# Kernel optimization log

Hardware: AMD Instinct MI355X
Metric: run time of the kernel (lower is better)

## Reference

```python
import jax, jax.numpy as jnp
import numpy as np

D_MODEL = 1024
NUM_HEADS = 16
HEAD_DIM = D_MODEL // NUM_HEADS


def setup_inputs() -> dict:
    key = jax.random.key(0)
    ks = jax.random.split(key, 5)
    x = jax.random.normal(ks[0], (4, 2048, D_MODEL), dtype=jnp.float32)
    # xavier_uniform with gain=0.1 for square (D,D) weights: limit = 0.1*sqrt(6/(D+D))
    limit = 0.1 * np.sqrt(6.0 / (2 * D_MODEL))
    def w(k):
        return jax.random.uniform(k, (D_MODEL, D_MODEL), jnp.float32, -limit, limit)
    return {
        "x": x,
        "W_q": w(ks[1]), "b_q": jnp.zeros((D_MODEL,), jnp.float32),
        "W_k": w(ks[2]), "b_k": jnp.zeros((D_MODEL,), jnp.float32),
        "W_v": w(ks[3]), "b_v": jnp.zeros((D_MODEL,), jnp.float32),
        "W_o": w(ks[4]), "b_o": jnp.zeros((D_MODEL,), jnp.float32),
    }


def reference(x, W_q, b_q, W_k, b_k, W_v, b_v, W_o, b_o):
    B, S, D = x.shape
    H, Hd = NUM_HEADS, HEAD_DIM
    # Linear: x @ W^T + b (torch nn.Linear convention); weights here are (out, in)
    def proj(W, b):
        y = jnp.einsum('bsd,ed->bse', x, W) + b
        return y.reshape(B, S, H, Hd).transpose(0, 2, 1, 3)  # [B,H,S,Hd]
    Q = proj(W_q, b_q)
    K = proj(W_k, b_k)
    V = proj(W_v, b_v)
    scale = 1.0 / np.sqrt(Hd).astype(np.float32)
    scores = jnp.einsum('bhqd,bhkd->bhqk', Q, K) * scale  # [B,H,S,S]
    attn = jax.nn.softmax(scores, axis=-1)
    ctx = jnp.einsum('bhqk,bhkd->bhqd', attn, V)
    ctx = ctx.transpose(0, 2, 1, 3).reshape(B, S, D)
    out = jnp.einsum('bsd,ed->bse', ctx, W_o) + b_o
    return out
```

## Files before the change

kernel.cpp:

```cpp
#include <hip/hip_runtime.h>
#include <math.h>

#define B_  4
#define S_  2048
#define D_  1024
#define H_  16
#define HD_ 64
#define M_  (B_*S_)

typedef short short8 __attribute__((ext_vector_type(8)));
typedef float f32x4 __attribute__((ext_vector_type(4)));

#define MFMA16(a,b,c) __builtin_amdgcn_mfma_f32_16x16x32_bf16(a, b, c, 0, 0, 0)

#if __has_builtin(__builtin_amdgcn_exp2f)
#define EXP2(x) __builtin_amdgcn_exp2f(x)
#else
#define EXP2(x) exp2f(x)
#endif

__device__ __forceinline__ unsigned short f2bf(float f) {
    unsigned u = __float_as_uint(f);
    u = (u + 0x7FFF + ((u >> 16) & 1)) >> 16;
    return (unsigned short)u;
}

__device__ __forceinline__ unsigned pack_bf16(float a, float b) {
#if __has_builtin(__builtin_amdgcn_cvt_pk_bf16_f32)
    typedef __bf16 bf2 __attribute__((ext_vector_type(2)));
    bf2 v = __builtin_amdgcn_cvt_pk_bf16_f32(a, b);
    unsigned r;
    __builtin_memcpy(&r, &v, 4);
    return r;
#else
    unsigned ua = __float_as_uint(a), ub = __float_as_uint(b);
    ua += 0x7FFFu + ((ua >> 16) & 1u);
    ub += 0x7FFFu + ((ub >> 16) & 1u);
    return __builtin_amdgcn_perm(ub, ua, 0x07060302u);
#endif
}

__device__ __forceinline__ void async_copy16(const void* g, void* l) {
    __builtin_amdgcn_global_load_lds(
        (const __attribute__((address_space(1))) void*)g,
        (__attribute__((address_space(3))) void*)l, 16, 0, 0);
}

#define VMW(n) asm volatile("s_waitcnt vmcnt(" #n ")" ::: "memory")
#define BARS() do { __builtin_amdgcn_s_barrier(); \
                    __builtin_amdgcn_sched_barrier(0); } while (0)

__global__ __launch_bounds__(256) void cvt_all(
    const float* __restrict__ x,
    const float* __restrict__ w0, const float* __restrict__ w1,
    const float* __restrict__ w2, const float* __restrict__ w3,
    unsigned short* __restrict__ xb, unsigned short* __restrict__ wb)
{
    size_t i = ((size_t)blockIdx.x * 256 + threadIdx.x) * 4;
    const float* src; unsigned short* dst;
    if (i < (size_t)M_ * D_) {
        src = x + i; dst = xb + i;
    } else {
        size_t j = i - (size_t)M_ * D_;
        int z = (int)(j >> 20);
        const float* w = (z == 0) ? w0 : (z == 1) ? w1 : (z == 2) ? w2 : w3;
        src = w + (j & ((size_t)D_ * D_ - 1)); dst = wb + j;
    }
    float4 v = *(const float4*)src;
    uint2 o;
    o.x = pack_bf16(v.x, v.y);
    o.y = pack_bf16(v.z, v.w);
    *(uint2*)dst = o;
}

__global__ __launch_bounds__(512, 2) void qkv256(
    const unsigned short* __restrict__ A,
    const unsigned short* __restrict__ W,
    const float* __restrict__ bq, const float* __restrict__ bk,
    const float* __restrict__ bv,
    unsigned short* __restrict__ Qo, unsigned short* __restrict__ Ko,
    unsigned short* __restrict__ Vo)
{
    __shared__ unsigned short As[2][256 * 64];
    __shared__ unsigned short Ws[2][256 * 64];
    const int K = D_;
    int tid = threadIdx.x;
    int w = tid >> 6, lane = tid & 63;
    int quad = lane >> 4, l16 = lane & 15;
    int r8 = lane >> 3, c8 = lane & 7;
    int cK = c8 ^ r8;
    int wm = w >> 2, wn = w & 3;
    int fl = l16 & 7;

    int lin = blockIdx.x + 12 * blockIdx.y;
    int swz = (lin & 7) * 48 + (lin >> 3);
    int by = swz / 12, bx = swz % 12;
    int m0 = by * 256, n0 = bx * 256;

    int z = bx >> 2;
    const float* bias = (z == 0) ? bq : (z == 1) ? bk : bv;
    unsigned short* out = (z == 0) ? Qo : (z == 1) ? Ko : Vo;
    float cscale = (z == 0) ? 0.125f * 1.44269504088896f : 1.0f;

    f32x4 acc[8][4];
    #pragma unroll
    for (int i = 0; i < 8; ++i)
        #pragma unroll
        for (int j = 0; j < 4; ++j)
            acc[i][j] = (f32x4){0.f, 0.f, 0.f, 0.f};

    const unsigned short* Ag = A + (size_t)(m0 + r8) * K + cK * 8;
    const unsigned short* Wg = W + (size_t)(n0 + r8) * K + cK * 8;

    auto stA = [&](int slot, int kt, int h) {
        #pragma unroll
        for (int ii = 0; ii < 2; ++ii) {
            int rb = ii * 128 + h * 64 + w * 8;
            async_copy16(Ag + (size_t)rb * K + kt * 64, &As[slot][rb * 64]);
        }
    };
    auto stB = [&](int slot, int kt, int h) {
        #pragma unroll
        for (int ii = 0; ii < 2; ++ii) {
            int rb = (ii * 2 + (w >> 2)) * 64 + h * 32 + (w & 3) * 8;
            async_copy16(Wg + (size_t)rb * K + kt * 64, &Ws[slot][rb * 64]);
        }
    };

    stA(0, 0, 0); stB(0, 0, 0); stB(0, 0, 1); stA(0, 0, 1);
    VMW(4);
    BARS();

    #define RD_A(i, off, s) (*(const short8*)&As[cur][(wm * 128 + (off) + (i) * 16 + l16) * 64 + \
                              (((quad + (s) * 4) ^ fl) * 8)])
    #define RD_B(j, off, s) (*(const short8*)&Ws[cur][(wn * 64 + (off) + (j) * 16 + l16) * 64 + \
                              (((quad + (s) * 4) ^ fl) * 8)])

    const int NT = K / 64;
    for (int kt = 0; kt < NT; ++kt) {
        int cur = kt & 1, nxt = cur ^ 1;
        bool pre = (kt + 1 < NT);
        short8 a[4][2], b0[2][2], b1[2][2];

        #pragma unroll
        for (int i = 0; i < 4; ++i)
            #pragma unroll
            for (int s = 0; s < 2; ++s) a[i][s] = RD_A(i, 0, s);
        #pragma unroll
        for (int j = 0; j < 2; ++j)
            #pragma unroll
            for (int s = 0; s < 2; ++s) b0[j][s] = RD_B(j, 0, s);
        if (pre) { stA(nxt, kt + 1, 0); VMW(4); } else VMW(2);
        BARS();
        #pragma unroll
        for (int i = 0; i < 4; ++i)
            #pragma unroll
            for (int j = 0; j < 2; ++j)
                #pragma unroll
                for (int s = 0; s < 2; ++s)
                    acc[i][j] = MFMA16(a[i][s], b0[j][s], acc[i][j]);

        #pragma unroll
        for (int j = 0; j < 2; ++j)
            #pragma unroll
            for (int s = 0; s < 2; ++s) b1[j][s] = RD_B(j, 32, s);
        if (pre) { stB(nxt, kt + 1, 0); VMW(4); } else VMW(0);
        BARS();
        #pragma unroll
        for (int i = 0; i < 4; ++i)
            #pragma unroll
            for (int j = 0; j < 2; ++j)
                #pragma unroll
                for (int s = 0; s < 2; ++s)
                    acc[i][j + 2] = MFMA16(a[i][s], b1[j][s], acc[i][j + 2]);

        #pragma unroll
        for (int i = 0; i < 4; ++i)
            #pragma unroll
            for (int s = 0; s < 2; ++s) a[i][s] = RD_A(i, 64, s);
        if (pre) stB(nxt, kt + 1, 1);
        BARS();
        #pragma unroll
        for (int i = 0; i < 4; ++i)
            #pragma unroll
            for (int j = 0; j < 2; ++j)
                #pragma unroll
                for (int s = 0; s < 2; ++s)
                    acc[i + 4][j + 2] = MFMA16(a[i][s], b1[j][s], acc[i + 4][j + 2]);

        if (pre) { stA(nxt, kt + 1, 1); VMW(4); }
        BARS();
        #pragma unroll
        for (int i = 0; i < 4; ++i)
            #pragma unroll
            for (int j = 0; j < 2; ++j)
                #pragma unroll
                for (int s = 0; s < 2; ++s)
                    acc[i + 4][j] = MFMA16(a[i][s], b0[j][s], acc[i + 4][j]);
    }
    #undef RD_A
    #undef RD_B

    #pragma unroll
    for (int ih = 0; ih < 2; ++ih)
    #pragma unroll
    for (int i = 0; i < 4; ++i) {
        int mb = m0 + wm * 128 + ih * 64 + i * 16 + quad * 4;
        #pragma unroll
        for (int j = 0; j < 4; ++j) {
            int n = n0 + wn * 64 + j * 16 + l16;
            int nn = n & 1023;
            float bn = bias[nn];
            int h = nn >> 6, hd = nn & 63;
            f32x4 v = acc[ih * 4 + i][j];
            if (z != 2) {
                #pragma unroll
                for (int r = 0; r < 4; ++r) {
                    int m = mb + r;
                    int bb = m >> 11, s = m & (S_ - 1);
                    out[(((size_t)(bb * H_ + h)) * S_ + s) * HD_ + hd] =
                        f2bf((v[r] + bn) * cscale);
                }
            } else {
                int bb = mb >> 11, s0 = mb & (S_ - 1);
                uint2 o;
                o.x = pack_bf16(v[0] + bn, v[1] + bn);
                o.y = pack_bf16(v[2] + bn, v[3] + bn);
                *(uint2*)&out[(((size_t)(bb * H_ + h)) * HD_ + hd) * S_ + s0] = o;
            }
        }
    }
}

__device__ __forceinline__ void gemm_body(
    const unsigned short* __restrict__ A, const unsigned short* __restrict__ W,
    const float* __restrict__ bias, void* __restrict__ out,
    int mode, float cscale, int bx, int by)
{
    __shared__ unsigned short As[2][128 * 64];
    __shared__ unsigned short Ws[2][128 * 64];
    const int K = D_;
    int tid = threadIdx.x;
    int w = tid >> 6, lane = tid & 63;
    int quad = lane >> 4, l16 = lane & 15;
    int r8 = lane >> 3, c8 = lane & 7;
    int cK = c8 ^ r8;
    int wm = w >> 2, wn = w & 3;
    int m0 = by * 128, n0 = bx * 128;
    int fl = l16 & 7;

    f32x4 acc[4][2];
    #pragma unroll
    for (int i = 0; i < 4; ++i)
        #pragma unroll
        for (int j = 0; j < 2; ++j)
            acc[i][j] = (f32x4){0.f, 0.f, 0.f, 0.f};

    const unsigned short* Ag = A + (size_t)(m0 + w * 16 + r8) * K + cK * 8;
    const unsigned short* Wg = W + (size_t)(n0 + w * 16 + r8) * K + cK * 8;

    auto stage = [&](int slot, int kt) {
        #pragma unroll
        for (int ii = 0; ii < 2; ++ii) {
            async_copy16(Ag + (size_t)(ii * 8) * K + kt * 64,
                         &As[slot][(w * 16 + ii * 8) * 64]);
            async_copy16(Wg + (size_t)(ii * 8) * K + kt * 64,
                         &Ws[slot][(w * 16 + ii * 8) * 64]);
        }
    };

    stage(0, 0);
    __syncthreads();

    const int NT = K / 64;
    for (int kt = 0; kt < NT; ++kt) {
        int cur = kt & 1;
        if (kt + 1 < NT) stage(cur ^ 1, kt + 1);

        #pragma unroll
        for (int s = 0; s < 2; ++s) {
            int st = ((quad + s * 4) ^ fl) * 8;
            short8 a[4], b[2];
            #pragma unroll
            for (int i = 0; i < 4; ++i)
                a[i] = *(const short8*)&As[cur][(wm * 64 + i * 16 + l16) * 64 + st];
            #pragma unroll
            for (int j = 0; j < 2; ++j)
                b[j] = *(const short8*)&Ws[cur][(wn * 32 + j * 16 + l16) * 64 + st];
            #pragma unroll
            for (int i = 0; i < 4; ++i)
                #pragma unroll
                for (int j = 0; j < 2; ++j)
                    acc[i][j] = MFMA16(a[i], b[j], acc[i][j]);
        }

        asm volatile("s_waitcnt vmcnt(0)" ::: "memory");
        __builtin_amdgcn_s_barrier();
        __builtin_amdgcn_sched_barrier(0);
    }

    #pragma unroll
    for (int i = 0; i < 4; ++i) {
        int mb = m0 + wm * 64 + i * 16 + quad * 4;
        #pragma unroll
        for (int j = 0; j < 2; ++j) {
            int n = n0 + wn * 32 + j * 16 + l16;
            float bn = bias[n];
            if (mode == 0) {
                #pragma unroll
                for (int r = 0; r < 4; ++r)
                    ((float*)out)[(size_t)(mb + r) * D_ + n] = acc[i][j][r] + bn;
            }
        }
    }
}

__global__ __launch_bounds__(512, 4) void out_gemm(
    const unsigned short* __restrict__ A, const unsigned short* __restrict__ W,
    const float* __restrict__ bias, float* __restrict__ out)
{
    int lin = blockIdx.x + 8 * blockIdx.y;
    int swz = (lin & 7) * 64 + (lin >> 3);
    gemm_body(A, W, bias, out, 0, 1.0f, swz & 7, swz >> 3);
}

__global__ __launch_bounds__(512, 4) void attn_mfma(
    const unsigned short* __restrict__ Q, const unsigned short* __restrict__ K,
    const unsigned short* __restrict__ VT, unsigned short* __restrict__ ctx)
{
    __shared__ unsigned short Ks[3 * 64 * 64];
    __shared__ unsigned short VTs[3 * 64 * 64];
    __shared__ unsigned short QPs[256 * 64];

    int tid = threadIdx.x;
    int w = tid >> 6, lane = tid & 63;
    int quad = lane >> 4, l16 = lane & 15;
    int r8 = lane >> 3, c8 = lane & 7;
    int cK = c8 ^ r8;
    int fl  = l16 & 7;
    int fl2 = (l16 ^ (l16 >> 1)) & 7;
    int bh = blockIdx.x;
    int q0 = blockIdx.y * 256;

    const unsigned short* Qp = Q + ((size_t)bh * S_ + q0) * HD_;
    const unsigned short* Kp = K + (size_t)bh * S_ * HD_;
    const unsigned short* Vp = VT + (size_t)bh * HD_ * S_;

    int cQ = c8 ^ r8 ^ (r8 >> 1) ^ ((w & 1) * 4);
    #pragma unroll
    for (int ii = 0; ii < 4; ++ii)
        async_copy16(Qp + (size_t)(ii * 64 + w * 8 + r8) * HD_ + cQ * 8,
                     QPs + (ii * 64 + w * 8) * 64);
    #pragma unroll
    for (int t = 0; t < 2; ++t) {
        async_copy16(Kp + (size_t)(t * 64 + w * 8 + r8) * HD_ + cK * 8,
                     Ks + t * 4096 + (w * 8) * 64);
        async_copy16(Vp + (size_t)(w * 8 + r8) * S_ + t * 64 + cK * 8,
                     VTs + t * 4096 + (w * 8) * 64);
    }
    __syncthreads();

    short8 bq_[2][2];
    #pragma unroll
    for (int mt = 0; mt < 2; ++mt)
        #pragma unroll
        for (int s = 0; s < 2; ++s)
            bq_[mt][s] = *(const short8*)&QPs[(w * 32 + mt * 16 + l16) * 64 +
                                              (((quad + s * 4) ^ fl2) * 8)];

    f32x4 O[2][4];
    float lsum[2] = {0.f, 0.f};
    #pragma unroll
    for (int mt = 0; mt < 2; ++mt)
        #pragma unroll
        for (int nt = 0; nt < 4; ++nt) O[mt][nt] = (f32x4){0.f, 0.f, 0.f, 0.f};

    const int NT = S_ / 64;
    for (int kt = 0; kt < NT; ++kt) {
        if (kt + 2 < NT) {
            int nb = ((kt + 2) % 3) * 4096;
            async_copy16(Kp + (size_t)((kt + 2) * 64 + w * 8 + r8) * HD_ + cK * 8,
                         Ks + nb + (w * 8) * 64);
            async_copy16(Vp + (size_t)(w * 8 + r8) * S_ + (kt + 2) * 64 + cK * 8,
                         VTs + nb + (w * 8) * 64);
        }
        const unsigned short* ks  = Ks + (kt % 3) * 4096;
        const unsigned short* vts = VTs + (kt % 3) * 4096;

        f32x4 sc[2][4];
        #pragma unroll
        for (int mt = 0; mt < 2; ++mt)
            #pragma unroll
            for (int nt = 0; nt < 4; ++nt) sc[mt][nt] = (f32x4){0.f, 0.f, 0.f, 0.f};
        #pragma unroll
        for (int s = 0; s < 2; ++s) {
            int stk = ((quad + s * 4) ^ fl) * 8;
            #pragma unroll
            for (int nt = 0; nt < 4; ++nt) {
                short8 ak = *(const short8*)&ks[(nt * 16 + l16) * 64 + stk];
                sc[0][nt] = MFMA16(ak, bq_[0][s], sc[0][nt]);
                sc[1][nt] = MFMA16(ak, bq_[1][s], sc[1][nt]);
            }
        }

        #pragma unroll
        for (int mt = 0; mt < 2; ++mt) {
            #pragma unroll
            for (int nt = 0; nt < 4; ++nt) {
                float p0 = EXP2(sc[mt][nt][0]);
                float p1 = EXP2(sc[mt][nt][1]);
                float p2 = EXP2(sc[mt][nt][2]);
                float p3 = EXP2(sc[mt][nt][3]);
                lsum[mt] += (p0 + p1) + (p2 + p3);
                uint2 pk;
                pk.x = pack_bf16(p0, p1);
                pk.y = pack_bf16(p2, p3);
                int addr = (w * 32 + mt * 16 + l16) * 64 +
                           (((nt * 2 + (quad >> 1)) ^ fl2) * 8) + (quad & 1) * 4;
                *(uint2*)&QPs[addr] = pk;
            }
        }

        #pragma unroll
        for (int s = 0; s < 2; ++s) {
            int stp = ((quad + s * 4) ^ fl2) * 8;
            int stv = ((quad + s * 4) ^ fl) * 8;
            short8 pa0 = *(const short8*)&QPs[(w * 32 + l16) * 64 + stp];
            short8 pa1 = *(const short8*)&QPs[(w * 32 + 16 + l16) * 64 + stp];
            #pragma unroll
            for (int nt = 0; nt < 4; ++nt) {
                short8 bv_ = *(const short8*)&vts[(nt * 16 + l16) * 64 + stv];
                O[0][nt] = MFMA16(pa0, bv_, O[0][nt]);
                O[1][nt] = MFMA16(pa1, bv_, O[1][nt]);
            }
        }

        if (kt + 2 < NT) asm volatile("s_waitcnt vmcnt(2)" ::: "memory");
        else             asm volatile("s_waitcnt vmcnt(0)" ::: "memory");
        __builtin_amdgcn_s_barrier();
        __builtin_amdgcn_sched_barrier(0);
    }

    float linv[2];
    #pragma unroll
    for (int mt = 0; mt < 2; ++mt) {
        float l = lsum[mt];
        l += __shfl_xor(l, 16);
        l += __shfl_xor(l, 32);
        linv[mt] = 1.0f / l;
    }

    int b = bh >> 4, h = bh & (H_ - 1);
    #pragma unroll
    for (int mt = 0; mt < 2; ++mt)
        #pragma unroll
        for (int r = 0; r < 4; ++r) {
            float inv = __shfl(linv[mt], quad * 4 + r, 64);
            int q = q0 + w * 32 + mt * 16 + quad * 4 + r;
            size_t base = ((size_t)(b * S_) + q) * D_ + h * HD_;
            #pragma unroll
            for (int nt = 0; nt < 4; ++nt)
                ctx[base + nt * 16 + l16] = f2bf(O[mt][nt][r] * inv);
        }
}

extern "C" void kernel_launch(void* const* d_in, const int* in_sizes, int n_in,
                              void* d_out, int out_size, void* d_ws, size_t ws_size,
                              hipStream_t stream) {
    const float* x  = (const float*)d_in[0];
    const float* Wq = (const float*)d_in[1];
    const float* bq = (const float*)d_in[2];
    const float* Wk = (const float*)d_in[3];
    const float* bk = (const float*)d_in[4];
    const float* Wv = (const float*)d_in[5];
    const float* bv = (const float*)d_in[6];
    const float* Wo = (const float*)d_in[7];
    const float* bo = (const float*)d_in[8];

    unsigned short* xb  = (unsigned short*)d_ws;
    unsigned short* wb  = xb + (size_t)M_ * D_;
    unsigned short* Qb  = wb + (size_t)4 * D_ * D_;
    unsigned short* Kb  = Qb + (size_t)M_ * D_;
    unsigned short* VTb = Kb + (size_t)M_ * D_;
    unsigned short* ctb = VTb + (size_t)M_ * D_;

    int cvt_blocks = (M_ * D_ + 4 * D_ * D_) / 1024;
    cvt_all<<<cvt_blocks, 256, 0, stream>>>(x, Wq, Wk, Wv, Wo, xb, wb);

    qkv256<<<dim3(12, 32), 512, 0, stream>>>(
        xb, wb, bq, bk, bv, Qb, Kb, VTb);

    attn_mfma<<<dim3(B_ * H_, S_ / 256), 512, 0, stream>>>(Qb, Kb, VTb, ctb);

    out_gemm<<<dim3(D_ / 128, M_ / 128), 512, 0, stream>>>(
        ctb, wb + (size_t)3 * D_ * D_, bo, (float*)d_out);
}
```

Measured before the change: 269.1 us.

## Halve attention query tile to 128 rows with double-buffered K/V

The attention kernel now gives each block 128 query rows instead of 256, so each wave handles one 16-row MFMA tile instead of two. The K/V shared-memory ring drops from three stages to two, and the wait before the barrier becomes a full vmcnt(0). The launch-bounds occupancy hint rises from 4 to 6, and the grid doubles. This trades lower LDS use and more blocks and occupancy for half the reuse of each K/V tile and each shared-memory fragment load, more global K/V traffic, and a shallower prefetch pipeline.

```diff
diff --git a/kernel.cpp b/kernel.cpp
--- a/kernel.cpp
+++ b/kernel.cpp
@@ -324,13 +324,13 @@
     gemm_body(A, W, bias, out, 0, 1.0f, swz & 7, swz >> 3);
 }
 
-__global__ __launch_bounds__(512, 4) void attn_mfma(
+__global__ __launch_bounds__(512, 6) void attn_mfma(
     const unsigned short* __restrict__ Q, const unsigned short* __restrict__ K,
     const unsigned short* __restrict__ VT, unsigned short* __restrict__ ctx)
 {
-    __shared__ unsigned short Ks[3 * 64 * 64];
-    __shared__ unsigned short VTs[3 * 64 * 64];
-    __shared__ unsigned short QPs[256 * 64];
+    __shared__ unsigned short Ks[2 * 64 * 64];
+    __shared__ unsigned short VTs[2 * 64 * 64];
+    __shared__ unsigned short QPs[128 * 64];
 
     int tid = threadIdx.x;
     int w = tid >> 6, lane = tid & 63;
@@ -340,7 +340,7 @@
     int fl  = l16 & 7;
     int fl2 = (l16 ^ (l16 >> 1)) & 7;
     int bh = blockIdx.x;
-    int q0 = blockIdx.y * 256;
+    int q0 = blockIdx.y * 128;
 
     const unsigned short* Qp = Q + ((size_t)bh * S_ + q0) * HD_;
     const unsigned short* Kp = K + (size_t)bh * S_ * HD_;
@@ -348,120 +348,98 @@
 
     int cQ = c8 ^ r8 ^ (r8 >> 1) ^ ((w & 1) * 4);
     #pragma unroll
-    for (int ii = 0; ii < 4; ++ii)
+    for (int ii = 0; ii < 2; ++ii)
         async_copy16(Qp + (size_t)(ii * 64 + w * 8 + r8) * HD_ + cQ * 8,
                      QPs + (ii * 64 + w * 8) * 64);
-    #pragma unroll
-    for (int t = 0; t < 2; ++t) {
-        async_copy16(Kp + (size_t)(t * 64 + w * 8 + r8) * HD_ + cK * 8,
-                     Ks + t * 4096 + (w * 8) * 64);
-        async_copy16(Vp + (size_t)(w * 8 + r8) * S_ + t * 64 + cK * 8,
-                     VTs + t * 4096 + (w * 8) * 64);
-    }
+    async_copy16(Kp + (size_t)(w * 8 + r8) * HD_ + cK * 8, Ks + (w * 8) * 64);
+    async_copy16(Vp + (size_t)(w * 8 + r8) * S_ + cK * 8, VTs + (w * 8) * 64);
     __syncthreads();
 
-    short8 bq_[2][2];
-    #pragma unroll
-    for (int mt = 0; mt < 2; ++mt)
-        #pragma unroll
-        for (int s = 0; s < 2; ++s)
-            bq_[mt][s] = *(const short8*)&QPs[(w * 32 + mt * 16 + l16) * 64 +
-                                              (((quad + s * 4) ^ fl2) * 8)];
-
-    f32x4 O[2][4];
-    float lsum[2] = {0.f, 0.f};
-    #pragma unroll
-    for (int mt = 0; mt < 2; ++mt)
-        #pragma unroll
-        for (int nt = 0; nt < 4; ++nt) O[mt][nt] = (f32x4){0.f, 0.f, 0.f, 0.f};
+    short8 bq_[2];
+    #pragma unroll
+    for (int s = 0; s < 2; ++s)
+        bq_[s] = *(const short8*)&QPs[(w * 16 + l16) * 64 +
+                                      (((quad + s * 4) ^ fl2) * 8)];
+
+    f32x4 O[4];
+    float lsum = 0.f;
+    #pragma unroll
+    for (int nt = 0; nt < 4; ++nt) O[nt] = (f32x4){0.f, 0.f, 0.f, 0.f};
 
     const int NT = S_ / 64;
+    int cur = 0;
     for (int kt = 0; kt < NT; ++kt) {
-        if (kt + 2 < NT) {
-            int nb = ((kt + 2) % 3) * 4096;
-            async_copy16(Kp + (size_t)((kt + 2) * 64 + w * 8 + r8) * HD_ + cK * 8,
+        if (kt + 1 < NT) {
+            int nb = (cur ^ 1) * 4096;
+            async_copy16(Kp + (size_t)((kt + 1) * 64 + w * 8 + r8) * HD_ + cK * 8,
                          Ks + nb + (w * 8) * 64);
-            async_copy16(Vp + (size_t)(w * 8 + r8) * S_ + (kt + 2) * 64 + cK * 8,
+            async_copy16(Vp + (size_t)(w * 8 + r8) * S_ + (kt + 1) * 64 + cK * 8,
                          VTs + nb + (w * 8) * 64);
         }
-        const unsigned short* ks  = Ks + (kt % 3) * 4096;
-        const unsigned short* vts = VTs + (kt % 3) * 4096;
-
-        f32x4 sc[2][4];
-        #pragma unroll
-        for (int mt = 0; mt < 2; ++mt)
-            #pragma unroll
-            for (int nt = 0; nt < 4; ++nt) sc[mt][nt] = (f32x4){0.f, 0.f, 0.f, 0.f};
+        const unsigned short* ks  = Ks + cur * 4096;
+        const unsigned short* vts = VTs + cur * 4096;
+
+        f32x4 sc[4];
+        #pragma unroll
+        for (int nt = 0; nt < 4; ++nt) sc[nt] = (f32x4){0.f, 0.f, 0.f, 0.f};
         #pragma unroll
         for (int s = 0; s < 2; ++s) {
             int stk = ((quad + s * 4) ^ fl) * 8;
             #pragma unroll
             for (int nt = 0; nt < 4; ++nt) {
                 short8 ak = *(const short8*)&ks[(nt * 16 + l16) * 64 + stk];
-                sc[0][nt] = MFMA16(ak, bq_[0][s], sc[0][nt]);
-                sc[1][nt] = MFMA16(ak, bq_[1][s], sc[1][nt]);
+                sc[nt] = MFMA16(ak, bq_[s], sc[nt]);
             }
         }
 
         #pragma unroll
-        for (int mt = 0; mt < 2; ++mt) {
-            #pragma unroll
-            for (int nt = 0; nt < 4; ++nt) {
-                float p0 = EXP2(sc[mt][nt][0]);
-                float p1 = EXP2(sc[mt][nt][1]);
-                float p2 = EXP2(sc[mt][nt][2]);
-                float p3 = EXP2(sc[mt][nt][3]);
-                lsum[mt] += (p0 + p1) + (p2 + p3);
-                uint2 pk;
-                pk.x = pack_bf16(p0, p1);
-                pk.y = pack_bf16(p2, p3);
-                int addr = (w * 32 + mt * 16 + l16) * 64 +
-                           (((nt * 2 + (quad >> 1)) ^ fl2) * 8) + (quad & 1) * 4;
-                *(uint2*)&QPs[addr] = pk;
-            }
+        for (int nt = 0; nt < 4; ++nt) {
+            float p0 = EXP2(sc[nt][0]);
+            float p1 = EXP2(sc[nt][1]);
+            float p2 = EXP2(sc[nt][2]);
+            float p3 = EXP2(sc[nt][3]);
+            lsum += (p0 + p1) + (p2 + p3);
+            uint2 pk;
+            pk.x = pack_bf16(p0, p1);
+            pk.y = pack_bf16(p2, p3);
+            int addr = (w * 16 + l16) * 64 +
+                       (((nt * 2 + (quad >> 1)) ^ fl2) * 8) + (quad & 1) * 4;
+            *(uint2*)&QPs[addr] = pk;
         }
 
         #pragma unroll
         for (int s = 0; s < 2; ++s) {
             int stp = ((quad + s * 4) ^ fl2) * 8;
             int stv = ((quad + s * 4) ^ fl) * 8;
-            short8 pa0 = *(const short8*)&QPs[(w * 32 + l16) * 64 + stp];
-            short8 pa1 = *(const short8*)&QPs[(w * 32 + 16 + l16) * 64 + stp];
+            short8 pa = *(const short8*)&QPs[(w * 16 + l16) * 64 + stp];
             #pragma unroll
             for (int nt = 0; nt < 4; ++nt) {
                 short8 bv_ = *(const short8*)&vts[(nt * 16 + l16) * 64 + stv];
-                O[0][nt] = MFMA16(pa0, bv_, O[0][nt]);
-                O[1][nt] = MFMA16(pa1, bv_, O[1][nt]);
+                O[nt] = MFMA16(pa, bv_, O[nt]);
             }
         }
 
-        if (kt + 2 < NT) asm volatile("s_waitcnt vmcnt(2)" ::: "memory");
-        else             asm volatile("s_waitcnt vmcnt(0)" ::: "memory");
+        asm volatile("s_waitcnt vmcnt(0)" ::: "memory");
         __builtin_amdgcn_s_barrier();
         __builtin_amdgcn_sched_barrier(0);
-    }
-
-    float linv[2];
-    #pragma unroll
-    for (int mt = 0; mt < 2; ++mt) {
-        float l = lsum[mt];
-        l += __shfl_xor(l, 16);
-        l += __shfl_xor(l, 32);
-        linv[mt] = 1.0f / l;
-    }
+        cur ^= 1;
+    }
+
+    float l = lsum;
+    l += __shfl_xor(l, 16);
+    l += __shfl_xor(l, 32);
+    float linv = 1.0f / l;
 
     int b = bh >> 4, h = bh & (H_ - 1);
     #pragma unroll
-    for (int mt = 0; mt < 2; ++mt)
-        #pragma unroll
-        for (int r = 0; r < 4; ++r) {
-            float inv = __shfl(linv[mt], quad * 4 + r, 64);
-            int q = q0 + w * 32 + mt * 16 + quad * 4 + r;
-            size_t base = ((size_t)(b * S_) + q) * D_ + h * HD_;
-            #pragma unroll
-            for (int nt = 0; nt < 4; ++nt)
-                ctx[base + nt * 16 + l16] = f2bf(O[mt][nt][r] * inv);
-        }
+    for (int r = 0; r < 4; ++r) {
+        float inv = __shfl(linv, quad * 4 + r, 64);
+        int q = q0 + w * 16 + quad * 4 + r;
+        size_t base = ((size_t)(b * S_) + q) * D_ + h * HD_;
+        #pragma unroll
+        for (int nt = 0; nt < 4; ++nt)
+            ctx[base + nt * 16 + l16] = f2bf(O[nt][r] * inv);
+    }
 }
 
 extern "C" void kernel_launch(void* const* d_in, const int* in_sizes, int n_in,
@@ -490,7 +468,7 @@
     qkv256<<<dim3(12, 32), 512, 0, stream>>>(
         xb, wb, bq, bk, bv, Qb, Kb, VTb);
 
-    attn_mfma<<<dim3(B_ * H_, S_ / 256), 512, 0, stream>>>(Qb, Kb, VTb, ctb);
+    attn_mfma<<<dim3(B_ * H_, S_ / 128), 512, 0, stream>>>(Qb, Kb, VTb, ctb);
 
     out_gemm<<<dim3(D_ / 128, M_ / 128), 512, 0, stream>>>(
         ctb, wb + (size_t)3 * D_ * D_, bo, (float*)d_out);
```

Result: slower. 285.7 us (+6.2%).

## Restructure QKV GEMM main loop barriers with setprio and remap out_gemm tiles

Applied to the files above, without the earlier changes.

The QKV projection GEMM loop now issues the next tile's async copies before the barrier and waits on LDS reads with lgkmcnt(0). The vmcnt waits move to after each MFMA phase, and each MFMA cluster is wrapped in s_setprio(1)/s_setprio(0). The aim is to overlap global-to-LDS copies with MFMA work and give the compute phases scheduling priority across waves. The out_gemm block-to-tile mapping also changes so that each XCD handles a contiguous group of row tiles, for better L2 locality. The extra barriers per iteration add synchronisation overhead.

```diff
diff --git a/kernel.cpp b/kernel.cpp
--- a/kernel.cpp
+++ b/kernel.cpp
@@ -46,9 +46,10 @@
         (__attribute__((address_space(3))) void*)l, 16, 0, 0);
 }
 
-#define VMW(n) asm volatile("s_waitcnt vmcnt(" #n ")" ::: "memory")
-#define BARS() do { __builtin_amdgcn_s_barrier(); \
-                    __builtin_amdgcn_sched_barrier(0); } while (0)
+#define VMW(n)  asm volatile("s_waitcnt vmcnt(" #n ")" ::: "memory")
+#define LGKM0() asm volatile("s_waitcnt lgkmcnt(0)" ::: "memory")
+#define BAR()   __builtin_amdgcn_s_barrier()
+#define SCH0()  __builtin_amdgcn_sched_barrier(0)
 
 __global__ __launch_bounds__(256) void cvt_all(
     const float* __restrict__ x,
@@ -129,7 +130,7 @@
 
     stA(0, 0, 0); stB(0, 0, 0); stB(0, 0, 1); stA(0, 0, 1);
     VMW(4);
-    BARS();
+    BAR(); SCH0();
 
     #define RD_A(i, off, s) (*(const short8*)&As[cur][(wm * 128 + (off) + (i) * 16 + l16) * 64 + \
                               (((quad + (s) * 4) ^ fl) * 8)])
@@ -150,8 +151,9 @@
         for (int j = 0; j < 2; ++j)
             #pragma unroll
             for (int s = 0; s < 2; ++s) b0[j][s] = RD_B(j, 0, s);
-        if (pre) { stA(nxt, kt + 1, 0); VMW(4); } else VMW(2);
-        BARS();
+        if (pre) stA(nxt, kt + 1, 0);
+        BAR(); LGKM0(); SCH0();
+        __builtin_amdgcn_s_setprio(1);
         #pragma unroll
         for (int i = 0; i < 4; ++i)
             #pragma unroll
@@ -159,13 +161,17 @@
                 #pragma unroll
                 for (int s = 0; s < 2; ++s)
                     acc[i][j] = MFMA16(a[i][s], b0[j][s], acc[i][j]);
+        __builtin_amdgcn_s_setprio(0);
+        if (pre) VMW(4); else VMW(2);
+        BAR(); SCH0();
 
         #pragma unroll
         for (int j = 0; j < 2; ++j)
             #pragma unroll
             for (int s = 0; s < 2; ++s) b1[j][s] = RD_B(j, 32, s);
-        if (pre) { stB(nxt, kt + 1, 0); VMW(4); } else VMW(0);
-        BARS();
+        if (pre) stB(nxt, kt + 1, 0);
+        BAR(); LGKM0(); SCH0();
+        __builtin_amdgcn_s_setprio(1);
         #pragma unroll
         for (int i = 0; i < 4; ++i)
             #pragma unroll
@@ -173,13 +179,17 @@
                 #pragma unroll
                 for (int s = 0; s < 2; ++s)
                     acc[i][j + 2] = MFMA16(a[i][s], b1[j][s], acc[i][j + 2]);
+        __builtin_amdgcn_s_setprio(0);
+        if (pre) VMW(4); else VMW(0);
+        BAR(); SCH0();
 
         #pragma unroll
         for (int i = 0; i < 4; ++i)
             #pragma unroll
             for (int s = 0; s < 2; ++s) a[i][s] = RD_A(i, 64, s);
         if (pre) stB(nxt, kt + 1, 1);
-        BARS();
+        BAR(); LGKM0(); SCH0();
+        __builtin_amdgcn_s_setprio(1);
         #pragma unroll
         for (int i = 0; i < 4; ++i)
             #pragma unroll
@@ -187,9 +197,11 @@
                 #pragma unroll
                 for (int s = 0; s < 2; ++s)
                     acc[i + 4][j + 2] = MFMA16(a[i][s], b1[j][s], acc[i + 4][j + 2]);
-
-        if (pre) { stA(nxt, kt + 1, 1); VMW(4); }
-        BARS();
+        __builtin_amdgcn_s_setprio(0);
+        BAR(); SCH0();
+
+        if (pre) stA(nxt, kt + 1, 1);
+        __builtin_amdgcn_s_setprio(1);
         #pragma unroll
         for (int i = 0; i < 4; ++i)
             #pragma unroll
@@ -197,6 +209,9 @@
                 #pragma unroll
                 for (int s = 0; s < 2; ++s)
                     acc[i + 4][j] = MFMA16(a[i][s], b0[j][s], acc[i + 4][j]);
+        __builtin_amdgcn_s_setprio(0);
+        if (pre) VMW(4);
+        BAR(); SCH0();
     }
     #undef RD_A
     #undef RD_B
@@ -320,8 +335,10 @@
     const float* __restrict__ bias, float* __restrict__ out)
 {
     int lin = blockIdx.x + 8 * blockIdx.y;
-    int swz = (lin & 7) * 64 + (lin >> 3);
-    gemm_body(A, W, bias, out, 0, 1.0f, swz & 7, swz >> 3);
+    int xcd = lin & 7, c = lin >> 3;
+    int by = xcd * 8 + (c & 7);
+    int bx = c >> 3;
+    gemm_body(A, W, bias, out, 0, 1.0f, bx, by);
 }
 
 __global__ __launch_bounds__(512, 4) void attn_mfma(
```

New measurement: 269.2 us. About the same (+0.0%).
